# Kernel tuning notes

Hardware: AMD Instinct MI355X
Metric: run time of the kernel (lower is better)

## Reference

```python
import jax, jax.numpy as jnp
import numpy as np

N, E, K = 50000, 1_000_000, 512
C, HALF, L, HID, NT = 64, 32, 16, 1024, 11
EPS = 1e-5


def _bn(x, gamma, beta):
    # BatchNorm1d in training mode: biased batch stats over node axis
    m = x.mean(axis=0)
    v = x.var(axis=0)
    return gamma * (x - m) * jax.lax.rsqrt(v + EPS) + beta


def _biconv(x, src, dst, w, n):
    # adjacency @ x  ->  out_i = sum_{(j->i) in edges} x_j  (edge (src=j, dst=i))
    out = jax.ops.segment_sum(x[src], dst, num_segments=n) @ w[0]
    # adjacency_t @ x -> scatter along src
    back = jax.ops.segment_sum(x[dst], src, num_segments=n) @ w[1]
    return jnp.concatenate([out, back], axis=1)  # [n, C]


def setup_inputs() -> dict:
    key = jax.random.key(0)
    ks = jax.random.split(key, 12)
    return {
        "node_types": jax.random.randint(ks[0], (N,), 0, NT, dtype=jnp.int32),
        "edge_index": jax.random.randint(ks[1], (2, E), 0, N, dtype=jnp.int32),
        "indices": jax.random.randint(ks[2], (K,), 0, N, dtype=jnp.int32),
        "emb": jax.random.normal(ks[3], (NT, C), dtype=jnp.float32),
        "conv0_w": jax.random.normal(ks[4], (2, C, HALF), dtype=jnp.float32) * 0.18,
        "res_bn_gamma": jnp.ones((L, 2, C), dtype=jnp.float32),
        "res_bn_beta": jnp.zeros((L, 2, C), dtype=jnp.float32),
        "res_w": jax.random.normal(ks[5], (L, 2, 2, C, HALF), dtype=jnp.float32) * 0.18,
        "hidden_w": jax.random.normal(ks[6], (18 * C, HID), dtype=jnp.float32) * 0.03,
        "hidden_b": jnp.zeros((HID,), dtype=jnp.float32),
        "out_w": jax.random.normal(ks[7], (HID, 1), dtype=jnp.float32) * 0.03,
        "out_b": jnp.zeros((1,), dtype=jnp.float32),
    }


def reference(node_types, edge_index, indices, emb, conv0_w, res_bn_gamma,
              res_bn_beta, res_w, hidden_w, hidden_b, out_w, out_b):
    n = node_types.shape[0]
    src, dst = edge_index[0], edge_index[1]

    x = emb[node_types]                       # [N, C] embedding lookup
    log0 = x
    x = _biconv(x, src, dst, conv0_w, n)      # conv0
    log1 = x

    def step(x, p):
        gamma, beta, w = p                    # [2,C], [2,C], [2,2,C,HALF]
        skip = x
        h = _bn(jax.nn.relu(x), gamma[0], beta[0])
        h = _biconv(h, src, dst, w[0], n)
        h = _bn(jax.nn.relu(h), gamma[1], beta[1])
        h = _biconv(h, src, dst, w[1], n)
        x = skip + h
        return x, x

    _, ys = jax.lax.scan(step, x, (res_bn_gamma, res_bn_beta, res_w))  # ys [L,N,C]

    full = jnp.concatenate(
        [log0, log1, ys.transpose(1, 0, 2).reshape(n, L * C)], axis=1)  # [N, 18*C]
    sel = full[indices]                        # [K, 18*C]
    h = jax.nn.relu(sel) @ hidden_w + hidden_b
    o = (jax.nn.relu(h) @ out_w + out_b).squeeze(-1)  # [K]
    return jax.nn.softmax(o, axis=0)
```

## Files before the change

### kernel.cpp

```cpp
#include <hip/hip_runtime.h>
#include <hip/hip_fp16.h>

#define NN 50000
#define NE 1000000
#define CC 64
#define LL 16
#define KSEL 512
#define HIDD 1024
#define FULLW 1152
#define EPSV 1e-5f
#define SBLK 49


__global__ __launch_bounds__(256) void hist_kernel(const int* __restrict__ src,
    const int* __restrict__ dst, int* __restrict__ cnt_in, int* __restrict__ cnt_out) {
  int stride = gridDim.x * blockDim.x;
  for (int e = blockIdx.x * blockDim.x + threadIdx.x; e < NE; e += stride) {
    atomicAdd(&cnt_in[dst[e]], 1);
    atomicAdd(&cnt_out[src[e]], 1);
  }
}


__global__ __launch_bounds__(1024) void scan1_kernel(const int* __restrict__ cnt,
    int* __restrict__ rptmp, int* __restrict__ btot) {
  int a = blockIdx.x / SBLK, blk = blockIdx.x % SBLK;
  int t = threadIdx.x;
  int idx = blk * 1024 + t;
  int v = (idx < NN) ? cnt[a * NN + idx] : 0;
  __shared__ int sm[1024];
  sm[t] = v;
  __syncthreads();
  for (int off = 1; off < 1024; off <<= 1) {
    int u = (t >= off) ? sm[t - off] : 0;
    __syncthreads();
    sm[t] += u;
    __syncthreads();
  }
  int incl = sm[t];
  if (idx < NN) rptmp[a * NN + idx] = incl - v;
  if (t == 1023) btot[a * SBLK + blk] = incl;
}

__global__ __launch_bounds__(256) void scan2_kernel(int* __restrict__ btot) {
  __shared__ int sm[256];
  int t = threadIdx.x;
  for (int a = 0; a < 2; ++a) {
    int v = (t < SBLK) ? btot[a * SBLK + t] : 0;
    sm[t] = v;
    __syncthreads();
    for (int off = 1; off < 256; off <<= 1) {
      int u = (t >= off) ? sm[t - off] : 0;
      __syncthreads();
      sm[t] += u;
      __syncthreads();
    }
    if (t < SBLK) btot[a * SBLK + t] = sm[t] - v;
    __syncthreads();
  }
}

__global__ __launch_bounds__(256) void scan3_kernel(const int* __restrict__ rptmp,
    const int* __restrict__ btot, int* __restrict__ rp, int* __restrict__ cur,
    float* __restrict__ statsA, int* __restrict__ inv) {
  int gid = blockIdx.x * 256 + threadIdx.x;
  if (gid < 2 * NN) {
    int a = gid / NN, idx = gid - a * NN;
    int v = rptmp[gid] + btot[a * SBLK + (idx >> 10)];
    rp[a * (NN + 1) + idx] = v;
    cur[gid] = v;
    if (idx == 0) rp[a * (NN + 1) + NN] = NE;
  }
  if (gid < NN) inv[gid] = -1;
  if (gid < 128) statsA[gid] = 0.f;
}


__global__ __launch_bounds__(256) void fill_kernel(const int* __restrict__ src,
    const int* __restrict__ dst, int* __restrict__ cur_in, int* __restrict__ cur_out,
    int* __restrict__ col_in, int* __restrict__ col_out,
    const int* __restrict__ indices, int* __restrict__ inv) {
  int gid = blockIdx.x * blockDim.x + threadIdx.x;
  if (gid < KSEL) atomicMax(&inv[indices[gid]], gid);
  int stride = gridDim.x * blockDim.x;
  for (int e = gid; e < NE; e += stride) {
    int s = src[e], d = dst[e];
    int p = atomicAdd(&cur_in[d], 1);
    col_in[p] = s;
    int q = atomicAdd(&cur_out[s], 1);
    col_out[q] = d;
  }
}


__global__ __launch_bounds__(256) void embed_kernel(const int* __restrict__ nt,
    const float* __restrict__ emb, float* __restrict__ X,
    const int* __restrict__ inv, float* __restrict__ sel) {
  int id = blockIdx.x * 256 + threadIdx.x;
  if (id >= NN * CC) return;
  int node = id >> 6, c = id & 63;
  float v = emb[nt[node] * CC + c];
  X[id] = v;
  int w = inv[node];
  if (w >= 0) sel[w * FULLW + c] = v;
}


__global__ __launch_bounds__(256) void fixup_kernel(const int* __restrict__ indices,
    const int* __restrict__ inv, float* __restrict__ sel) {
  int tid = blockIdx.x * 256 + threadIdx.x;
  if (tid >= KSEL * FULLW) return;
  int k = tid / FULLW, col = tid - k * FULLW;
  int w = inv[indices[k]];
  if (w != k) sel[k * FULLW + col] = sel[w * FULLW + col];
}


__global__ __launch_bounds__(256) void mm_kernel(const float* __restrict__ X,
    __half* __restrict__ Y, const float* __restrict__ W,
    const float* __restrict__ stats, const float* __restrict__ gamma,
    const float* __restrict__ beta, float* __restrict__ stats_zero) {
  int t = threadIdx.x;
  int lane = t & 63;
  int wid = t >> 6;
  float wreg[CC];
  {
    const float* wb = W + (lane >> 5) * 2048 + (lane & 31);
#pragma unroll
    for (int c2 = 0; c2 < CC; ++c2) wreg[c2] = wb[c2 * 32];
  }
  __shared__ float sc[CC], sh[CC];
  __shared__ __align__(16) float Xs[64][CC];
  if (t < CC) {
    float scale = 1.f, shift = 0.f;
    if (stats) {
      float m = stats[t] * (1.f / NN);
      float v = stats[CC + t] * (1.f / NN) - m * m;
      float is = rsqrtf(v + EPSV);
      scale = gamma[t] * is;
      shift = beta[t] - m * scale;
    }
    sc[t] = scale; sh[t] = shift;
  }
  if (stats_zero && blockIdx.x == 0 && t < 128) stats_zero[t] = 0.f;
  const bool bn = (stats != nullptr);
  for (int row0 = blockIdx.x * 64; row0 < NN; row0 += gridDim.x * 64) {
    int nrows = min(64, NN - row0);
    __syncthreads();
    for (int idx = t; idx < nrows * 16; idx += 256) {
      int r = idx >> 4, cq = idx & 15;
      float4 v = *(const float4*)(X + (size_t)(row0 + r) * CC + cq * 4);
      if (bn) {
        int c0 = cq * 4;
        v.x = fmaxf(v.x, 0.f) * sc[c0]     + sh[c0];
        v.y = fmaxf(v.y, 0.f) * sc[c0 + 1] + sh[c0 + 1];
        v.z = fmaxf(v.z, 0.f) * sc[c0 + 2] + sh[c0 + 2];
        v.w = fmaxf(v.w, 0.f) * sc[c0 + 3] + sh[c0 + 3];
      }
      *(float4*)&Xs[r][cq * 4] = v;
    }
    __syncthreads();
    for (int r = wid; r < nrows; r += 4) {
      const float* xr = &Xs[r][0];
      float a0 = 0.f, a1 = 0.f, a2 = 0.f, a3 = 0.f;
#pragma unroll
      for (int c2 = 0; c2 < CC; c2 += 4) {
        float4 xv = *(const float4*)(xr + c2);
        a0 += xv.x * wreg[c2];
        a1 += xv.y * wreg[c2 + 1];
        a2 += xv.z * wreg[c2 + 2];
        a3 += xv.w * wreg[c2 + 3];
      }
      Y[(size_t)(row0 + r) * CC + lane] = __float2half((a0 + a1) + (a2 + a3));
    }
  }
}


__global__ __launch_bounds__(256) void seg_kernel(
    const __half* __restrict__ Y, const float* skip, float* OUT,
    const int* __restrict__ rp_in, const int* __restrict__ col_in,
    const int* __restrict__ rp_out, const int* __restrict__ col_out,
    float* __restrict__ stats_acc,
    const int* __restrict__ inv, float* __restrict__ sel, int coloff) {
  int t = threadIdx.x;
  int c = t & 63;
  int local = t >> 6;
  const int* rp = (c < 32) ? rp_in : rp_out;
  const int* col = (c < 32) ? col_in : col_out;
  float s1 = 0.f, s2 = 0.f;
  for (int i0 = blockIdx.x * 4; i0 < NN; i0 += gridDim.x * 4) {
    int i = i0 + local;
    if (i < NN) {
      int beg = rp[i], end = rp[i + 1];
      float a0 = 0.f, a1 = 0.f, a2 = 0.f, a3 = 0.f;
      float a4 = 0.f, a5 = 0.f, a6 = 0.f, a7 = 0.f;
      int e = beg;
      for (; e + 8 <= end; e += 8) {
        int j0 = col[e], j1 = col[e + 1], j2 = col[e + 2], j3 = col[e + 3];
        int j4 = col[e + 4], j5 = col[e + 5], j6 = col[e + 6], j7 = col[e + 7];
        a0 += __half2float(Y[j0 * CC + c]);
        a1 += __half2float(Y[j1 * CC + c]);
        a2 += __half2float(Y[j2 * CC + c]);
        a3 += __half2float(Y[j3 * CC + c]);
        a4 += __half2float(Y[j4 * CC + c]);
        a5 += __half2float(Y[j5 * CC + c]);
        a6 += __half2float(Y[j6 * CC + c]);
        a7 += __half2float(Y[j7 * CC + c]);
      }
      if (e + 4 <= end) {
        int j0 = col[e], j1 = col[e + 1], j2 = col[e + 2], j3 = col[e + 3];
        a0 += __half2float(Y[j0 * CC + c]);
        a1 += __half2float(Y[j1 * CC + c]);
        a2 += __half2float(Y[j2 * CC + c]);
        a3 += __half2float(Y[j3 * CC + c]);
        e += 4;
      }
      if (e + 2 <= end) {
        int j0 = col[e], j1 = col[e + 1];
        a4 += __half2float(Y[j0 * CC + c]);
        a5 += __half2float(Y[j1 * CC + c]);
        e += 2;
      }
      if (e < end) a6 += __half2float(Y[col[e] * CC + c]);
      float acc = ((a0 + a1) + (a2 + a3)) + ((a4 + a5) + (a6 + a7));
      if (skip) acc += skip[i * CC + c];
      OUT[i * CC + c] = acc;
      if (coloff >= 0) {
        int w = inv[i];
        if (w >= 0) sel[w * FULLW + coloff + c] = acc;
      }
      float r = fmaxf(acc, 0.f);
      s1 += r; s2 += r * r;
    }
  }
  if (stats_acc) {
    __shared__ float red1[256], red2[256];
    red1[t] = s1; red2[t] = s2;
    __syncthreads();
    if (t < 64) {
      float v1 = red1[t] + red1[t + 64] + red1[t + 128] + red1[t + 192];
      float v2 = red2[t] + red2[t + 64] + red2[t + 128] + red2[t + 192];
      atomicAdd(&stats_acc[t], v1);
      atomicAdd(&stats_acc[CC + t], v2);
    }
  }
}


__global__ __launch_bounds__(256) void hidden_kernel(const float* __restrict__ sel,
    const float* __restrict__ Wh, const float* __restrict__ bh, float* __restrict__ h1) {
  int t = threadIdx.x;
  int lane = t & 63, w = t >> 6;
  int jb = blockIdx.x & 15;
  int rbg = blockIdx.x >> 4;
  int j = jb * 64 + lane;
  int r0 = rbg * 16;
  __shared__ __align__(16) float Ws[64][64];
  __shared__ __align__(16) float Ss[16][64];
  float acc[4] = {0.f, 0.f, 0.f, 0.f};
  for (int k0 = 0; k0 < FULLW; k0 += 64) {
    __syncthreads();
    {
      int col = (t & 15) * 4;
      int kk = t >> 4;
#pragma unroll
      for (int p = 0; p < 4; ++p) {
        float4 v = *(const float4*)(Wh + (size_t)(k0 + kk + p * 16) * HIDD + jb * 64 + col);
        *(float4*)&Ws[kk + p * 16][col] = v;
      }
      float4 v = *(const float4*)(sel + (size_t)(r0 + kk) * FULLW + k0 + col);
      v.x = fmaxf(v.x, 0.f); v.y = fmaxf(v.y, 0.f);
      v.z = fmaxf(v.z, 0.f); v.w = fmaxf(v.w, 0.f);
      *(float4*)&Ss[kk][col] = v;
    }
    __syncthreads();
    float wreg[64];
#pragma unroll
    for (int kk = 0; kk < 64; ++kk) wreg[kk] = Ws[kk][lane];
#pragma unroll
    for (int rr = 0; rr < 4; ++rr) {
      const float4* sr = (const float4*)&Ss[w * 4 + rr][0];
      float a0 = 0.f, a1 = 0.f, a2 = 0.f, a3 = 0.f;
#pragma unroll
      for (int kq = 0; kq < 16; ++kq) {
        float4 sv = sr[kq];
        a0 += sv.x * wreg[kq * 4];
        a1 += sv.y * wreg[kq * 4 + 1];
        a2 += sv.z * wreg[kq * 4 + 2];
        a3 += sv.w * wreg[kq * 4 + 3];
      }
      acc[rr] += (a0 + a1) + (a2 + a3);
    }
  }
#pragma unroll
  for (int rr = 0; rr < 4; ++rr)
    h1[(size_t)(r0 + w * 4 + rr) * HIDD + j] = acc[rr] + bh[j];
}

__global__ __launch_bounds__(256) void out_kernel(const float* __restrict__ h1,
    const float* __restrict__ ow, const float* __restrict__ ob, float* __restrict__ logits) {
  int k = blockIdx.x * 4 + (threadIdx.x >> 6);
  int lane = threadIdx.x & 63;
  if (k >= KSEL) return;
  float a = 0.f;
  for (int j = lane; j < HIDD; j += 64) {
    float v = h1[k * HIDD + j];
    a += fmaxf(v, 0.f) * ow[j];
  }
  for (int off = 32; off; off >>= 1) a += __shfl_down(a, off, 64);
  if (lane == 0) logits[k] = a + ob[0];
}

__global__ __launch_bounds__(512) void softmax_kernel(const float* __restrict__ logits,
    float* __restrict__ out) {
  int t = threadIdx.x;
  float v = logits[t];
  __shared__ float red[512];
  red[t] = v;
  __syncthreads();
  for (int s = 256; s; s >>= 1) { if (t < s) red[t] = fmaxf(red[t], red[t + s]); __syncthreads(); }
  float mx = red[0];
  __syncthreads();
  float e = expf(v - mx);
  red[t] = e;
  __syncthreads();
  for (int s = 256; s; s >>= 1) { if (t < s) red[t] += red[t + s]; __syncthreads(); }
  out[t] = e / red[0];
}


extern "C" void kernel_launch(void* const* d_in, const int* in_sizes, int n_in,
                              void* d_out, int out_size, void* d_ws, size_t ws_size,
                              hipStream_t stream) {
  const int* node_types = (const int*)d_in[0];
  const int* edge_index = (const int*)d_in[1];
  const int* indices = (const int*)d_in[2];
  const float* emb = (const float*)d_in[3];
  const float* conv0_w = (const float*)d_in[4];
  const float* bn_g = (const float*)d_in[5];
  const float* bn_b = (const float*)d_in[6];
  const float* res_w = (const float*)d_in[7];
  const float* hw = (const float*)d_in[8];
  const float* hb = (const float*)d_in[9];
  const float* ow = (const float*)d_in[10];
  const float* ob = (const float*)d_in[11];
  float* out = (float*)d_out;
  const int* src = edge_index;
  const int* dst = edge_index + NE;

  char* p = (char*)d_ws;
  size_t off = 0;
  auto alloc = [&](size_t bytes) -> void* {
    void* q = p + off;
    off += (bytes + 255) & ~(size_t)255;
    return q;
  };
  int* cnt = (int*)alloc(2 * NN * sizeof(int));
  int* rptmp = (int*)alloc(2 * NN * sizeof(int));
  int* btot = (int*)alloc(2 * SBLK * sizeof(int));
  int* rp = (int*)alloc(2 * (NN + 1) * sizeof(int));
  int* cur = (int*)alloc(2 * NN * sizeof(int));
  int* inv = (int*)alloc(NN * sizeof(int));
  int* col_in = (int*)alloc((size_t)NE * sizeof(int));
  int* col_out = (int*)alloc((size_t)NE * sizeof(int));
  float* X = (float*)alloc((size_t)NN * CC * 4);
  float* H = (float*)alloc((size_t)NN * CC * 4);
  __half* Y = (__half*)alloc((size_t)NN * CC * 2);
  float* statsA = (float*)alloc(128 * 4);
  float* statsB = (float*)alloc(128 * 4);
  float* sel = (float*)alloc((size_t)KSEL * FULLW * 4);
  float* h1 = (float*)alloc((size_t)KSEL * HIDD * 4);
  float* logits = (float*)alloc(KSEL * 4);
  (void)ws_size; (void)in_sizes; (void)n_in; (void)out_size;

  int* cnt_in = cnt;  int* cnt_out = cnt + NN;
  int* rp_in = rp;    int* rp_out = rp + NN + 1;
  int* cur_in = cur;  int* cur_out = cur + NN;

  hipMemsetAsync(cnt, 0, 2 * NN * sizeof(int), stream);
  hipLaunchKernelGGL(hist_kernel, dim3(1024), dim3(256), 0, stream, src, dst, cnt_in, cnt_out);
  hipLaunchKernelGGL(scan1_kernel, dim3(2 * SBLK), dim3(1024), 0, stream, cnt, rptmp, btot);
  hipLaunchKernelGGL(scan2_kernel, dim3(1), dim3(256), 0, stream, btot);
  hipLaunchKernelGGL(scan3_kernel, dim3((2 * NN + 255) / 256), dim3(256), 0, stream,
                     rptmp, btot, rp, cur, statsA, inv);
  hipLaunchKernelGGL(fill_kernel, dim3(1024), dim3(256), 0, stream, src, dst,
                     cur_in, cur_out, col_in, col_out, indices, inv);

  hipLaunchKernelGGL(embed_kernel, dim3((NN * CC + 255) / 256), dim3(256), 0, stream,
                     node_types, emb, X, inv, sel);

  hipLaunchKernelGGL(mm_kernel, dim3(782), dim3(256), 0, stream, X, Y, conv0_w,
                     (const float*)nullptr, (const float*)nullptr, (const float*)nullptr,
                     (float*)nullptr);
  hipLaunchKernelGGL(seg_kernel, dim3(2048), dim3(256), 0, stream, Y, (const float*)nullptr, X,
                     rp_in, col_in, rp_out, col_out, statsA, inv, sel, CC);

  for (int l = 0; l < LL; ++l) {
    const float* w1 = res_w + (size_t)(l * 2 + 0) * 4096;
    const float* w2 = res_w + (size_t)(l * 2 + 1) * 4096;
    const float* g1 = bn_g + (l * 2 + 0) * CC;
    const float* b1 = bn_b + (l * 2 + 0) * CC;
    const float* g2 = bn_g + (l * 2 + 1) * CC;
    const float* b2 = bn_b + (l * 2 + 1) * CC;
    hipLaunchKernelGGL(mm_kernel, dim3(782), dim3(256), 0, stream, X, Y, w1, statsA, g1, b1, statsB);
    hipLaunchKernelGGL(seg_kernel, dim3(2048), dim3(256), 0, stream, Y, (const float*)nullptr, H,
                       rp_in, col_in, rp_out, col_out, statsB,
                       (const int*)nullptr, (float*)nullptr, -1);
    hipLaunchKernelGGL(mm_kernel, dim3(782), dim3(256), 0, stream, H, Y, w2, statsB, g2, b2, statsA);
    hipLaunchKernelGGL(seg_kernel, dim3(2048), dim3(256), 0, stream, Y, X, X,
                       rp_in, col_in, rp_out, col_out, statsA, inv, sel, 2 * CC + l * CC);
  }

  hipLaunchKernelGGL(fixup_kernel, dim3((KSEL * FULLW + 255) / 256), dim3(256), 0, stream,
                     indices, inv, sel);
  hipLaunchKernelGGL(hidden_kernel, dim3(512), dim3(256), 0, stream, sel, hw, hb, h1);
  hipLaunchKernelGGL(out_kernel, dim3(KSEL / 4), dim3(256), 0, stream, h1, ow, ob, logits);
  hipLaunchKernelGGL(softmax_kernel, dim3(1), dim3(512), 0, stream, logits, out);
}
```

Baseline: 3.709 ms.

## Fold batchnorm into mm weights and use per-wave row tiles without block sync

Batchnorm scale is folded into the per-lane weight registers, and the shift becomes a bias computed once per lane, so the load loop only applies relu. The block-wide grid-stride loop with two __syncthreads per tile is replaced by each wave owning a private 16-row shared tile with no barriers. This removes shared-memory scale/shift lookups and block synchronisation. In exchange every thread recomputes 64 BN coefficients, and the kernel now assumes one 64-row tile per block, so the launch grid must cover all rows.

```diff
diff --git a/kernel.cpp b/kernel.cpp
--- a/kernel.cpp
+++ b/kernel.cpp
@@ -123,56 +123,55 @@
   int t = threadIdx.x;
   int lane = t & 63;
   int wid = t >> 6;
+  const bool bn = (stats != nullptr);
   float wreg[CC];
+  float shift = 0.f;
   {
     const float* wb = W + (lane >> 5) * 2048 + (lane & 31);
-#pragma unroll
-    for (int c2 = 0; c2 < CC; ++c2) wreg[c2] = wb[c2 * 32];
-  }
-  __shared__ float sc[CC], sh[CC];
-  __shared__ __align__(16) float Xs[64][CC];
-  if (t < CC) {
-    float scale = 1.f, shift = 0.f;
-    if (stats) {
-      float m = stats[t] * (1.f / NN);
-      float v = stats[CC + t] * (1.f / NN) - m * m;
-      float is = rsqrtf(v + EPSV);
-      scale = gamma[t] * is;
-      shift = beta[t] - m * scale;
-    }
-    sc[t] = scale; sh[t] = shift;
+    if (bn) {
+#pragma unroll
+      for (int c = 0; c < CC; ++c) {
+        float m = stats[c] * (1.f / NN);
+        float v = stats[CC + c] * (1.f / NN) - m * m;
+        float is = rsqrtf(v + EPSV);
+        float scale = gamma[c] * is;
+        float sh = beta[c] - m * scale;
+        float w = wb[c * 32];
+        wreg[c] = w * scale;
+        shift += sh * w;
+      }
+    } else {
+#pragma unroll
+      for (int c = 0; c < CC; ++c) wreg[c] = wb[c * 32];
+    }
   }
   if (stats_zero && blockIdx.x == 0 && t < 128) stats_zero[t] = 0.f;
-  const bool bn = (stats != nullptr);
-  for (int row0 = blockIdx.x * 64; row0 < NN; row0 += gridDim.x * 64) {
-    int nrows = min(64, NN - row0);
-    __syncthreads();
-    for (int idx = t; idx < nrows * 16; idx += 256) {
-      int r = idx >> 4, cq = idx & 15;
-      float4 v = *(const float4*)(X + (size_t)(row0 + r) * CC + cq * 4);
-      if (bn) {
-        int c0 = cq * 4;
-        v.x = fmaxf(v.x, 0.f) * sc[c0]     + sh[c0];
-        v.y = fmaxf(v.y, 0.f) * sc[c0 + 1] + sh[c0 + 1];
-        v.z = fmaxf(v.z, 0.f) * sc[c0 + 2] + sh[c0 + 2];
-        v.w = fmaxf(v.w, 0.f) * sc[c0 + 3] + sh[c0 + 3];
-      }
-      *(float4*)&Xs[r][cq * 4] = v;
-    }
-    __syncthreads();
-    for (int r = wid; r < nrows; r += 4) {
-      const float* xr = &Xs[r][0];
-      float a0 = 0.f, a1 = 0.f, a2 = 0.f, a3 = 0.f;
-#pragma unroll
-      for (int c2 = 0; c2 < CC; c2 += 4) {
-        float4 xv = *(const float4*)(xr + c2);
-        a0 += xv.x * wreg[c2];
-        a1 += xv.y * wreg[c2 + 1];
-        a2 += xv.z * wreg[c2 + 2];
-        a3 += xv.w * wreg[c2 + 3];
-      }
-      Y[(size_t)(row0 + r) * CC + lane] = __float2half((a0 + a1) + (a2 + a3));
-    }
+  __shared__ __align__(16) float Xs[4][16][CC];
+  int row0 = blockIdx.x * 64 + wid * 16;
+  if (row0 >= NN) return;
+  int nrows = min(16, NN - row0);
+  for (int idx = lane; idx < nrows * 16; idx += 64) {
+    int r = idx >> 4, cq = idx & 15;
+    float4 v = *(const float4*)(X + (size_t)(row0 + r) * CC + cq * 4);
+    if (bn) {
+      v.x = fmaxf(v.x, 0.f); v.y = fmaxf(v.y, 0.f);
+      v.z = fmaxf(v.z, 0.f); v.w = fmaxf(v.w, 0.f);
+    }
+    *(float4*)&Xs[wid][r][cq * 4] = v;
+  }
+  for (int r = 0; r < nrows; ++r) {
+    const float* xr = &Xs[wid][r][0];
+    float a0 = 0.f, a1 = 0.f, a2 = 0.f, a3 = 0.f;
+#pragma unroll
+    for (int c2 = 0; c2 < CC; c2 += 4) {
+      float4 xv = *(const float4*)(xr + c2);
+      a0 += xv.x * wreg[c2];
+      a1 += xv.y * wreg[c2 + 1];
+      a2 += xv.z * wreg[c2 + 2];
+      a3 += xv.w * wreg[c2 + 3];
+    }
+    Y[(size_t)(row0 + r) * CC + lane] =
+        __float2half(((a0 + a1) + (a2 + a3)) + shift);
   }
 }
 
```

Result: slower. 3.818 ms (+2.9%).
